# Kernel tuning notes

Hardware: AMD Instinct MI355X
Metric: run time of the kernel (lower is better)

## Reference

```python
import jax, jax.numpy as jnp
import numpy as np

USER_COUNT = 100000
ITEM_COUNT = 50000
N_NODES = USER_COUNT + ITEM_COUNT
EMB = 64
N_EDGES = 1250000
BATCH = 4096
GCN_LAYERS = 3


def setup_inputs() -> dict:
    key = jax.random.key(0)
    k = jax.random.split(key, 7)
    return {
        "user_emb": jax.random.normal(k[0], (USER_COUNT, EMB), dtype=jnp.float32) * 0.1,
        "item_emb": jax.random.normal(k[1], (ITEM_COUNT, EMB), dtype=jnp.float32) * 0.1,
        "edge_row": jax.random.randint(k[2], (N_EDGES,), 0, N_NODES, dtype=jnp.int32),
        "edge_col": jax.random.randint(k[3], (N_EDGES,), 0, N_NODES, dtype=jnp.int32),
        "edge_weight": jax.random.uniform(k[4], (N_EDGES,), dtype=jnp.float32) * 0.1,
        "users": jax.random.randint(k[5], (BATCH,), 0, USER_COUNT, dtype=jnp.int32),
        "items": jax.random.randint(k[6], (BATCH,), 0, ITEM_COUNT, dtype=jnp.int32),
    }


def reference(user_emb, item_emb, edge_row, edge_col, edge_weight, users, items):
    # ego = cat(user_emb, item_emb) : [N, d]
    ego = jnp.concatenate([user_emb, item_emb], axis=0)
    n = ego.shape[0]
    acc = ego  # running sum of hop embeddings (mean taken at the end)
    x = ego
    for _ in range(GCN_LAYERS):
        # SpMM: out[r] += w_e * x[c] for each edge e=(r,c)
        x = jax.ops.segment_sum(edge_weight[:, None] * x[edge_col], edge_row,
                                num_segments=n)
        acc = acc + x
    all_emb = acc / jnp.float32(GCN_LAYERS + 1)  # mean over stacked hops
    user_all = all_emb[:user_emb.shape[0]]
    item_all = all_emb[user_emb.shape[0]:]
    return (user_all[users], item_all[items])
```

## Files before the change

kernel.cpp:

```cpp
#include <hip/hip_runtime.h>

#define USER_COUNT 100000
#define ITEM_COUNT 50000
#define N_NODES    150000
#define EMB        64
#define N_EDGES    1250000
#define BATCH      4096

#define BROWS     512
#define NBKT      293
#define A1_TILE   2048
#define A1_BLOCKS ((N_EDGES + A1_TILE - 1) / A1_TILE)
#define PSTR      320
#define COLMASK   0x3FFFFu
#define ROW_ALLOC 150536
#define CSR_CAP   5120

#define CONCAT_BLOCKS 9375

static __device__ __forceinline__ unsigned pack_bf16x2(float a, float b) {
    unsigned ua = __float_as_uint(a);
    unsigned ub = __float_as_uint(b);
    ua += 0x7FFFu + ((ua >> 16) & 1u);
    ub += 0x7FFFu + ((ub >> 16) & 1u);
    return (ua >> 16) | (ub & 0xFFFF0000u);
}

static __device__ __forceinline__ const float* ego_ptr(unsigned c,
                                                       const float* __restrict__ ue,
                                                       const float* __restrict__ ie) {
    return (c < USER_COUNT) ? ue + (size_t)c * EMB
                            : ie + (size_t)(c - USER_COUNT) * EMB;
}

static __device__ __forceinline__ void fma4(float4& a, float w, uint2 p) {
    a.x += w * __uint_as_float(p.x << 16);
    a.y += w * __uint_as_float(p.x & 0xFFFF0000u);
    a.z += w * __uint_as_float(p.y << 16);
    a.w += w * __uint_as_float(p.y & 0xFFFF0000u);
}

static __device__ __forceinline__ float4 spmm_row16(const uint2* __restrict__ edges,
                                                    int s, int e,
                                                    const uint2* __restrict__ x2,
                                                    int l) {
    float4 a0 = {0.f,0.f,0.f,0.f}, a1 = {0.f,0.f,0.f,0.f};
    float4 a2 = {0.f,0.f,0.f,0.f}, a3 = {0.f,0.f,0.f,0.f};
    int i = s;
    for (; i + 7 < e; i += 8) {
        uint2 e0 = edges[i],     e1 = edges[i + 1];
        uint2 e2 = edges[i + 2], e3 = edges[i + 3];
        uint2 e4 = edges[i + 4], e5 = edges[i + 5];
        uint2 e6 = edges[i + 6], e7 = edges[i + 7];
        uint2 p0 = x2[(size_t)(e0.x & COLMASK) * 16 + l];
        uint2 p1 = x2[(size_t)(e1.x & COLMASK) * 16 + l];
        uint2 p2 = x2[(size_t)(e2.x & COLMASK) * 16 + l];
        uint2 p3 = x2[(size_t)(e3.x & COLMASK) * 16 + l];
        uint2 p4 = x2[(size_t)(e4.x & COLMASK) * 16 + l];
        uint2 p5 = x2[(size_t)(e5.x & COLMASK) * 16 + l];
        uint2 p6 = x2[(size_t)(e6.x & COLMASK) * 16 + l];
        uint2 p7 = x2[(size_t)(e7.x & COLMASK) * 16 + l];
        fma4(a0, __uint_as_float(e0.y), p0);
        fma4(a1, __uint_as_float(e1.y), p1);
        fma4(a2, __uint_as_float(e2.y), p2);
        fma4(a3, __uint_as_float(e3.y), p3);
        fma4(a0, __uint_as_float(e4.y), p4);
        fma4(a1, __uint_as_float(e5.y), p5);
        fma4(a2, __uint_as_float(e6.y), p6);
        fma4(a3, __uint_as_float(e7.y), p7);
    }
    if (i + 3 < e) {
        uint2 e0 = edges[i],     e1 = edges[i + 1];
        uint2 e2 = edges[i + 2], e3 = edges[i + 3];
        uint2 p0 = x2[(size_t)(e0.x & COLMASK) * 16 + l];
        uint2 p1 = x2[(size_t)(e1.x & COLMASK) * 16 + l];
        uint2 p2 = x2[(size_t)(e2.x & COLMASK) * 16 + l];
        uint2 p3 = x2[(size_t)(e3.x & COLMASK) * 16 + l];
        fma4(a0, __uint_as_float(e0.y), p0);
        fma4(a1, __uint_as_float(e1.y), p1);
        fma4(a2, __uint_as_float(e2.y), p2);
        fma4(a3, __uint_as_float(e3.y), p3);
        i += 4;
    }
    for (; i < e; ++i) {
        uint2 e0 = edges[i];
        uint2 p0 = x2[(size_t)(e0.x & COLMASK) * 16 + l];
        fma4(a0, __uint_as_float(e0.y), p0);
    }
    float4 r;
    r.x = (a0.x + a1.x) + (a2.x + a3.x);
    r.y = (a0.y + a1.y) + (a2.y + a3.y);
    r.z = (a0.z + a1.z) + (a2.z + a3.z);
    r.w = (a0.w + a1.w) + (a2.w + a3.w);
    return r;
}

__global__ void k_prep(const float* __restrict__ ue, const float* __restrict__ ie,
                       unsigned* __restrict__ x,
                       const int* __restrict__ row, int* __restrict__ partT) {
    __shared__ int h[PSTR];
    int tid = threadIdx.x;
    if (blockIdx.x < CONCAT_BLOCKS) {
        const size_t nu4 = (size_t)USER_COUNT * EMB / 4;
        size_t i = (size_t)blockIdx.x * 256 + tid;
        float4 v = (i < nu4) ? ((const float4*)ue)[i] : ((const float4*)ie)[i - nu4];
        uint2 p;
        p.x = pack_bf16x2(v.x, v.y);
        p.y = pack_bf16x2(v.z, v.w);
        ((uint2*)x)[i] = p;
    } else {
        int bb = blockIdx.x - CONCAT_BLOCKS;
        h[tid] = 0;
        if (tid + 256 < PSTR) h[tid + 256] = 0;
        __syncthreads();
        int base = bb * A1_TILE;
        #pragma unroll
        for (int j = 0; j < 8; ++j) {
            int e = base + j * 256 + tid;
            if (e < N_EDGES) atomicAdd(&h[row[e] >> 9], 1);
        }
        __syncthreads();
        if (tid < NBKT) partT[bb * PSTR + tid] = h[tid];
        if (tid + 256 < NBKT) partT[bb * PSTR + tid + 256] = h[tid + 256];
    }
}

__global__ void k_scanbkt(int* __restrict__ partT, int* __restrict__ gtot) {
    __shared__ int sA[256], sB[256];
    int t   = blockIdx.x;
    int tid = threadIdx.x;
    int v0 = 0, v1 = 0, v2 = 0;
    int b0 = tid * 3;
    if (b0 + 0 < A1_BLOCKS) v0 = partT[(b0 + 0) * PSTR + t];
    if (b0 + 1 < A1_BLOCKS) v1 = partT[(b0 + 1) * PSTR + t];
    if (b0 + 2 < A1_BLOCKS) v2 = partT[(b0 + 2) * PSTR + t];
    int s = v0 + v1 + v2;
    sA[tid] = s;
    __syncthreads();
    int* in = sA; int* out = sB;
    for (int off = 1; off < 256; off <<= 1) {
        out[tid] = in[tid] + ((tid >= off) ? in[tid - off] : 0);
        __syncthreads();
        int* tmp = in; in = out; out = tmp;
    }
    int run = in[tid] - s;
    if (b0 + 0 < A1_BLOCKS) { partT[(b0 + 0) * PSTR + t] = run; run += v0; }
    if (b0 + 1 < A1_BLOCKS) { partT[(b0 + 1) * PSTR + t] = run; run += v1; }
    if (b0 + 2 < A1_BLOCKS) { partT[(b0 + 2) * PSTR + t] = run; }
    if (tid == 255) gtot[t] = in[255];
}

__global__ void k_binfill(const int* __restrict__ row, const int* __restrict__ col,
                          const float* __restrict__ w,
                          const int* __restrict__ partT,
                          const int* __restrict__ gtot,
                          uint2* __restrict__ edges_a) {
    __shared__ int cnt[512], cnt2[PSTR], gpos[PSTR], sc[PSTR];
    __shared__ int sA[512], sB[512];
    __shared__ uint2 srec[A1_TILE];
    __shared__ int  sdst[A1_TILE];
    int tid = threadIdx.x;
    cnt[tid] = 0; cnt[tid + 256] = 0;
    cnt2[tid] = 0;
    if (tid + 256 < PSTR) cnt2[tid + 256] = 0;
    __syncthreads();

    int ebase   = blockIdx.x * A1_TILE;
    int tilecnt = min(A1_TILE, N_EDGES - ebase);

    int r[8], c[8]; float wv[8];
    #pragma unroll
    for (int j = 0; j < 8; ++j) {
        int e = ebase + j * 256 + tid;
        if (e < N_EDGES) {
            r[j] = row[e]; c[j] = col[e]; wv[j] = w[e];
            atomicAdd(&cnt[r[j] >> 9], 1);
        } else {
            r[j] = -1;
        }
    }
    __syncthreads();

    {
        int ga = (tid < NBKT) ? gtot[tid] : 0;
        int gb = (tid + 256 < NBKT) ? gtot[tid + 256] : 0;
        int* in = sA; int* out = sB;
        in[tid] = ga; in[tid + 256] = gb;
        __syncthreads();
        for (int off = 1; off < 512; off <<= 1) {
            out[tid] = in[tid] + ((tid >= off) ? in[tid - off] : 0);
            int i2 = tid + 256;
            out[i2] = in[i2] + ((i2 >= off) ? in[i2 - off] : 0);
            __syncthreads();
            int* t = in; in = out; out = t;
        }
        gpos[tid] = in[tid] - ga;
        if (tid + 256 < PSTR) gpos[tid + 256] = in[tid + 256] - gb;
    }
    __syncthreads();

    {
        int* in = sA; int* out = sB;
        in[tid] = cnt[tid]; in[tid + 256] = cnt[tid + 256];
        __syncthreads();
        for (int off = 1; off < 512; off <<= 1) {
            out[tid] = in[tid] + ((tid >= off) ? in[tid - off] : 0);
            int i2 = tid + 256;
            out[i2] = in[i2] + ((i2 >= off) ? in[i2 - off] : 0);
            __syncthreads();
            int* t = in; in = out; out = t;
        }
        #pragma unroll
        for (int k = 0; k < 2; ++k) {
            int b = tid + k * 256;
            if (b < NBKT) {
                sc[b]    = in[b] - cnt[b];
                gpos[b] += partT[blockIdx.x * PSTR + b];
            }
        }
    }
    __syncthreads();

    #pragma unroll
    for (int j = 0; j < 8; ++j) {
        if (r[j] >= 0) {
            int b  = r[j] >> 9;
            int lp = sc[b] + atomicAdd(&cnt2[b], 1);
            srec[lp] = make_uint2((unsigned)c[j] | ((unsigned)(r[j] & 511) << 18),
                                  __float_as_uint(wv[j]));
            sdst[lp] = gpos[b] + (lp - sc[b]);
        }
    }
    __syncthreads();

    #pragma unroll
    for (int j = 0; j < 8; ++j) {
        int i = j * 256 + tid;
        if (i < tilecnt) edges_a[sdst[i]] = srec[i];
    }
}

__global__ __launch_bounds__(512) void k_csrfill(const int* __restrict__ gtot,
                                                 const uint2* __restrict__ edges_a,
                                                 uint2* __restrict__ edges_b,
                                                 int* __restrict__ row_start) {
    __shared__ uint2 srec[CSR_CAP];
    __shared__ int hist[512], cur[512];
    __shared__ int sA[512], sB[512];
    __shared__ int sbase;
    int tid = threadIdx.x;
    int b   = blockIdx.x;

    {
        int ga = (tid < NBKT) ? gtot[tid] : 0;
        int* in = sA; int* out = sB;
        in[tid] = ga;
        if (tid < 256) { int gb = (tid + 256 < NBKT) ? gtot[tid + 256] : 0;
                         in[tid + 256] = gb; }
        __syncthreads();
        for (int off = 1; off < 512; off <<= 1) {
            out[tid] = in[tid] + ((tid >= off) ? in[tid - off] : 0);
            __syncthreads();
            int* t = in; in = out; out = t;
        }
        if (tid == 0) sbase = (b == 0) ? 0 : in[b - 1];
        __syncthreads();
    }
    int base  = sbase;
    int count = gtot[b];

    hist[tid] = 0;
    __syncthreads();
    for (int i = tid; i < count; i += 512) {
        uint2 rec = edges_a[base + i];
        if (i < CSR_CAP) srec[i] = rec;
        atomicAdd(&hist[(rec.x >> 18) & 511], 1);
    }
    __syncthreads();

    int hv = hist[tid];
    int* in = sA; int* out = sB;
    in[tid] = hv;
    __syncthreads();
    for (int off = 1; off < 512; off <<= 1) {
        out[tid] = in[tid] + ((tid >= off) ? in[tid - off] : 0);
        __syncthreads();
        int* t = in; in = out; out = t;
    }
    int excl = in[tid] - hv;
    row_start[b * BROWS + tid] = base + excl;
    cur[tid] = base + excl;
    __syncthreads();

    for (int i = tid; i < count; i += 512) {
        uint2 rec = (i < CSR_CAP) ? srec[i] : edges_a[base + i];
        int rl = (rec.x >> 18) & 511;
        int pos = atomicAdd(&cur[rl], 1);
        edges_b[pos] = rec;
    }
}

__global__ void k_spmm_bf16(const int* __restrict__ row_start,
                            const uint2* __restrict__ edges,
                            const uint2* __restrict__ xin2,
                            uint2* __restrict__ xout2) {
    int g = blockIdx.x * 16 + (threadIdx.x >> 4);
    int l = threadIdx.x & 15;
    if (g >= N_NODES) return;
    float4 a = spmm_row16(edges, row_start[g], row_start[g + 1], xin2, l);
    xout2[(size_t)g * 16 + l] = make_uint2(pack_bf16x2(a.x, a.y),
                                           pack_bf16x2(a.z, a.w));
}

__global__ void k_epilogue(const int* __restrict__ users,
                           const int* __restrict__ items,
                           const float* __restrict__ ue,
                           const float* __restrict__ ie,
                           const uint2* __restrict__ x1,
                           const uint2* __restrict__ x2,
                           const int* __restrict__ row_start,
                           const uint2* __restrict__ edges,
                           float* __restrict__ out) {
    int g = blockIdx.x * 16 + (threadIdx.x >> 4);
    int l = threadIdx.x & 15;
    if (g >= 2 * BATCH) return;
    int node = (g < BATCH) ? users[g] : USER_COUNT + items[g - BATCH];
    float4 l3 = spmm_row16(edges, row_start[node], row_start[node + 1], x2, l);
    float4 e = ((const float4*)ego_ptr((unsigned)node, ue, ie))[l];
    uint2 pa = x1[(size_t)node * 16 + l];
    uint2 pb = x2[(size_t)node * 16 + l];
    float4 r;
    r.x = 0.25f * (e.x + __uint_as_float(pa.x << 16)
                       + __uint_as_float(pb.x << 16)         + l3.x);
    r.y = 0.25f * (e.y + __uint_as_float(pa.x & 0xFFFF0000u)
                       + __uint_as_float(pb.x & 0xFFFF0000u) + l3.y);
    r.z = 0.25f * (e.z + __uint_as_float(pa.y << 16)
                       + __uint_as_float(pb.y << 16)         + l3.z);
    r.w = 0.25f * (e.w + __uint_as_float(pa.y & 0xFFFF0000u)
                       + __uint_as_float(pb.y & 0xFFFF0000u) + l3.w);
    ((float4*)out)[(size_t)g * 16 + l] = r;
}

extern "C" void kernel_launch(void* const* d_in, const int* in_sizes, int n_in,
                              void* d_out, int out_size, void* d_ws, size_t ws_size,
                              hipStream_t stream) {
    const float* user_emb    = (const float*)d_in[0];
    const float* item_emb    = (const float*)d_in[1];
    const int*   edge_row    = (const int*)d_in[2];
    const int*   edge_col    = (const int*)d_in[3];
    const float* edge_weight = (const float*)d_in[4];
    const int*   users       = (const int*)d_in[5];
    const int*   items       = (const int*)d_in[6];
    float* out = (float*)d_out;

    const size_t node_u32 = (size_t)N_NODES * 32;
    unsigned* xa        = (unsigned*)d_ws;
    unsigned* xb        = xa + node_u32;
    unsigned* xc        = xb + node_u32;
    int*      row_start = (int*)(xc + node_u32);
    int*      gtot      = row_start + ROW_ALLOC;
    int*      partT     = gtot + 512;
    uint2*    edges_a   = (uint2*)(partT + A1_BLOCKS * PSTR);
    uint2*    edges_b   = edges_a + N_EDGES;

    k_prep<<<CONCAT_BLOCKS + A1_BLOCKS, 256, 0, stream>>>(user_emb, item_emb,
                                                          xa, edge_row, partT);
    k_scanbkt<<<NBKT, 256, 0, stream>>>(partT, gtot);
    k_binfill<<<A1_BLOCKS, 256, 0, stream>>>(edge_row, edge_col, edge_weight,
                                             partT, gtot, edges_a);
    k_csrfill<<<NBKT, 512, 0, stream>>>(gtot, edges_a, edges_b, row_start);
    k_spmm_bf16<<<(N_NODES + 15) / 16, 256, 0, stream>>>(row_start, edges_b,
                                                         (const uint2*)xa,
                                                         (uint2*)xb);
    k_spmm_bf16<<<(N_NODES + 15) / 16, 256, 0, stream>>>(row_start, edges_b,
                                                         (const uint2*)xb,
                                                         (uint2*)xc);
    k_epilogue<<<(2 * BATCH + 15) / 16, 256, 0, stream>>>(users, items,
                                                          user_emb, item_emb,
                                                          (const uint2*)xb,
                                                          (const uint2*)xc,
                                                          row_start, edges_b,
                                                          out);
}
```

Before: 122.7 us.

## Move embedding concat into binfill and split csrfill buckets across two blocks

The bf16 concat/pack of the embeddings moves out of the histogram kernel and into the binfill launch as extra blocks. This shortens the histogram pass on the critical path and lets the concat overlap with the scatter. The CSR fill now launches two blocks per bucket, each owning half of the 512 local rows. That doubles parallelism for the under-occupied 293-block launch. In exchange each block reads the whole bucket twice and needs an extra atomic count to find where its half starts.

```diff
diff --git a/kernel.cpp b/kernel.cpp
--- a/kernel.cpp
+++ b/kernel.cpp
@@ -95,34 +95,22 @@
     return r;
 }
 
-__global__ void k_prep(const float* __restrict__ ue, const float* __restrict__ ie,
-                       unsigned* __restrict__ x,
-                       const int* __restrict__ row, int* __restrict__ partT) {
+__global__ void k_hist(const int* __restrict__ row, int* __restrict__ partT) {
     __shared__ int h[PSTR];
     int tid = threadIdx.x;
-    if (blockIdx.x < CONCAT_BLOCKS) {
-        const size_t nu4 = (size_t)USER_COUNT * EMB / 4;
-        size_t i = (size_t)blockIdx.x * 256 + tid;
-        float4 v = (i < nu4) ? ((const float4*)ue)[i] : ((const float4*)ie)[i - nu4];
-        uint2 p;
-        p.x = pack_bf16x2(v.x, v.y);
-        p.y = pack_bf16x2(v.z, v.w);
-        ((uint2*)x)[i] = p;
-    } else {
-        int bb = blockIdx.x - CONCAT_BLOCKS;
-        h[tid] = 0;
-        if (tid + 256 < PSTR) h[tid + 256] = 0;
-        __syncthreads();
-        int base = bb * A1_TILE;
-        #pragma unroll
-        for (int j = 0; j < 8; ++j) {
-            int e = base + j * 256 + tid;
-            if (e < N_EDGES) atomicAdd(&h[row[e] >> 9], 1);
-        }
-        __syncthreads();
-        if (tid < NBKT) partT[bb * PSTR + tid] = h[tid];
-        if (tid + 256 < NBKT) partT[bb * PSTR + tid + 256] = h[tid + 256];
-    }
+    int bb  = blockIdx.x;
+    h[tid] = 0;
+    if (tid + 256 < PSTR) h[tid + 256] = 0;
+    __syncthreads();
+    int base = bb * A1_TILE;
+    #pragma unroll
+    for (int j = 0; j < 8; ++j) {
+        int e = base + j * 256 + tid;
+        if (e < N_EDGES) atomicAdd(&h[row[e] >> 9], 1);
+    }
+    __syncthreads();
+    if (tid < NBKT) partT[bb * PSTR + tid] = h[tid];
+    if (tid + 256 < NBKT) partT[bb * PSTR + tid + 256] = h[tid + 256];
 }
 
 __global__ void k_scanbkt(int* __restrict__ partT, int* __restrict__ gtot) {
@@ -150,16 +138,32 @@
     if (tid == 255) gtot[t] = in[255];
 }
 
-__global__ void k_binfill(const int* __restrict__ row, const int* __restrict__ col,
-                          const float* __restrict__ w,
-                          const int* __restrict__ partT,
-                          const int* __restrict__ gtot,
-                          uint2* __restrict__ edges_a) {
+__global__ void k_binfill_concat(const int* __restrict__ row,
+                                 const int* __restrict__ col,
+                                 const float* __restrict__ w,
+                                 const int* __restrict__ partT,
+                                 const int* __restrict__ gtot,
+                                 uint2* __restrict__ edges_a,
+                                 const float* __restrict__ ue,
+                                 const float* __restrict__ ie,
+                                 unsigned* __restrict__ x) {
     __shared__ int cnt[512], cnt2[PSTR], gpos[PSTR], sc[PSTR];
     __shared__ int sA[512], sB[512];
     __shared__ uint2 srec[A1_TILE];
     __shared__ int  sdst[A1_TILE];
     int tid = threadIdx.x;
+
+    if (blockIdx.x >= A1_BLOCKS) {
+        const size_t nu4 = (size_t)USER_COUNT * EMB / 4;
+        size_t i = (size_t)(blockIdx.x - A1_BLOCKS) * 256 + tid;
+        float4 v = (i < nu4) ? ((const float4*)ue)[i] : ((const float4*)ie)[i - nu4];
+        uint2 p;
+        p.x = pack_bf16x2(v.x, v.y);
+        p.y = pack_bf16x2(v.z, v.w);
+        ((uint2*)x)[i] = p;
+        return;
+    }
+
     cnt[tid] = 0; cnt[tid + 256] = 0;
     cnt2[tid] = 0;
     if (tid + 256 < PSTR) cnt2[tid + 256] = 0;
@@ -245,11 +249,12 @@
                                                  uint2* __restrict__ edges_b,
                                                  int* __restrict__ row_start) {
     __shared__ uint2 srec[CSR_CAP];
-    __shared__ int hist[512], cur[512];
+    __shared__ int hist[256], cur[256];
     __shared__ int sA[512], sB[512];
-    __shared__ int sbase;
+    __shared__ int sbase, s_c0;
     int tid = threadIdx.x;
-    int b   = blockIdx.x;
+    int b   = blockIdx.x >> 1;
+    int h   = blockIdx.x & 1;
 
     {
         int ga = (tid < NBKT) ? gtot[tid] : 0;
@@ -263,39 +268,51 @@
             __syncthreads();
             int* t = in; in = out; out = t;
         }
-        if (tid == 0) sbase = (b == 0) ? 0 : in[b - 1];
+        if (tid == 0) { sbase = (b == 0) ? 0 : in[b - 1]; s_c0 = 0; }
         __syncthreads();
     }
     int base  = sbase;
     int count = gtot[b];
 
-    hist[tid] = 0;
-    __syncthreads();
+    if (tid < 256) { hist[tid] = 0; }
+    __syncthreads();
+
+    int c0 = 0;
     for (int i = tid; i < count; i += 512) {
         uint2 rec = edges_a[base + i];
         if (i < CSR_CAP) srec[i] = rec;
-        atomicAdd(&hist[(rec.x >> 18) & 511], 1);
-    }
-    __syncthreads();
-
-    int hv = hist[tid];
-    int* in = sA; int* out = sB;
-    in[tid] = hv;
-    __syncthreads();
-    for (int off = 1; off < 512; off <<= 1) {
-        out[tid] = in[tid] + ((tid >= off) ? in[tid - off] : 0);
-        __syncthreads();
-        int* t = in; in = out; out = t;
-    }
-    int excl = in[tid] - hv;
-    row_start[b * BROWS + tid] = base + excl;
-    cur[tid] = base + excl;
+        int rl = (rec.x >> 18) & 511;
+        c0 += (rl < 256);
+        if ((rl >> 8) == h) atomicAdd(&hist[rl & 255], 1);
+    }
+    if (c0) atomicAdd(&s_c0, c0);
+    __syncthreads();
+
+    int halfbase = base + (h ? s_c0 : 0);
+
+    {
+        int hv = (tid < 256) ? hist[tid] : 0;
+        int* in = sA; int* out = sB;
+        if (tid < 256) in[tid] = hv;
+        __syncthreads();
+        for (int off = 1; off < 256; off <<= 1) {
+            if (tid < 256) out[tid] = in[tid] + ((tid >= off) ? in[tid - off] : 0);
+            __syncthreads();
+            int* t = in; in = out; out = t;
+        }
+        if (tid < 256) {
+            int excl = in[tid] - hv;
+            row_start[b * BROWS + h * 256 + tid] = halfbase + excl;
+            cur[tid] = halfbase + excl;
+        }
+    }
     __syncthreads();
 
     for (int i = tid; i < count; i += 512) {
         uint2 rec = (i < CSR_CAP) ? srec[i] : edges_a[base + i];
         int rl = (rec.x >> 18) & 511;
-        int pos = atomicAdd(&cur[rl], 1);
+        if ((rl >> 8) != h) continue;
+        int pos = atomicAdd(&cur[rl & 255], 1);
         edges_b[pos] = rec;
     }
 }
@@ -363,12 +380,12 @@
     uint2*    edges_a   = (uint2*)(partT + A1_BLOCKS * PSTR);
     uint2*    edges_b   = edges_a + N_EDGES;
 
-    k_prep<<<CONCAT_BLOCKS + A1_BLOCKS, 256, 0, stream>>>(user_emb, item_emb,
-                                                          xa, edge_row, partT);
+    k_hist<<<A1_BLOCKS, 256, 0, stream>>>(edge_row, partT);
     k_scanbkt<<<NBKT, 256, 0, stream>>>(partT, gtot);
-    k_binfill<<<A1_BLOCKS, 256, 0, stream>>>(edge_row, edge_col, edge_weight,
-                                             partT, gtot, edges_a);
-    k_csrfill<<<NBKT, 512, 0, stream>>>(gtot, edges_a, edges_b, row_start);
+    k_binfill_concat<<<A1_BLOCKS + CONCAT_BLOCKS, 256, 0, stream>>>(
+        edge_row, edge_col, edge_weight, partT, gtot, edges_a,
+        user_emb, item_emb, xa);
+    k_csrfill<<<NBKT * 2, 512, 0, stream>>>(gtot, edges_a, edges_b, row_start);
     k_spmm_bf16<<<(N_NODES + 15) / 16, 256, 0, stream>>>(row_start, edges_b,
                                                          (const uint2*)xa,
                                                          (uint2*)xb);
```

Result: no change. 122.0 us (-0.5%).
